# Performance work log

Measured on AMD Instinct MI355X. Metric: run time of the kernel, lower is better.

## Reference

```python
import jax, jax.numpy as jnp
import numpy as np

N, C, H, W = 64, 256, 28, 28
INTER = 128  # in_channels // reduction
STD = 0.01   # init std of the 1x1 convs


def setup_inputs() -> dict:
    key = jax.random.key(0)
    k_x, k_idx, k_wq, k_wv, k_lam = jax.random.split(key, 5)
    x = jax.random.normal(k_x, (N, C, H, W), dtype=jnp.float32)
    lam = jax.random.uniform(k_lam, (), dtype=jnp.float32)
    index = jax.random.randint(k_idx, (N,), 0, N)
    # query 1x1 conv (shared for q and k since x_qk_concat=False -> key is None)
    Wq = jax.random.normal(k_wq, (INTER, C), dtype=jnp.float32) * STD
    bq = jnp.zeros((INTER,), dtype=jnp.float32)
    # value 1x1 conv -> 1 channel
    Wv = jax.random.normal(k_wv, (1, C), dtype=jnp.float32) * STD
    bv = jnp.zeros((1,), dtype=jnp.float32)
    return {"x": x, "lam": lam, "index": index, "Wq": Wq, "bq": bq,
            "Wv": Wv, "bv": bv, "scale_factor": 8}


def _conv1x1(x, w, b):
    # x: [n,c,h,w], w: [o,c], b: [o] -> [n,o,h,w]
    return jnp.einsum('nchw,oc->nohw', x, w) + b[None, :, None, None]


def reference(x, lam, index, Wq, bq, Wv, bv, scale_factor):
    n, c, h, w = x.shape
    hw = h * w
    x_lam = x               # [n,c,h,w]
    x_lam_ = x[index]       # shuffled pair
    # value: 1x1 conv to 1 channel -> [n, hw, 1]
    v = _conv1x1(x_lam_, Wv, bv).reshape(n, 1, hw).transpose(0, 2, 1)
    # query / key share the same conv (key is None when x_qk_concat=False)
    q = _conv1x1(x_lam, Wq, bq).reshape(n, INTER, hw).transpose(0, 2, 1)  # [n,hw,inter]
    k = _conv1x1(x_lam_, Wq, bq).reshape(n, INTER, hw)                    # [n,inter,hw]
    # embedded gaussian similarity, forced fp32, scaled by sqrt(inter)
    scores = jnp.einsum('nqc,nck->nqk', q.astype(jnp.float32), k.astype(jnp.float32))
    scores = scores / jnp.float32(np.sqrt(INTER))
    pw = jax.nn.softmax(scores, axis=-1)  # [n,hw,hw]
    mask = jnp.einsum('nqk,nko->nqo', pw, v.astype(jnp.float32)).reshape(n, 1, h, w)
    # bilinear upsample (align_corners=False semantics) then sigmoid
    mask = jax.image.resize(mask, (n, 1, h * scale_factor, w * scale_factor),
                            method='bilinear')
    mask = jax.nn.sigmoid(mask)
    # results['mask'] = cat([1 - m, m], dim=1)
    return jnp.concatenate([1.0 - mask, mask], axis=1)
```

## Files before the change

### kernel.cpp

```cpp
#include <hip/hip_runtime.h>
#include <math.h>

#define NB    64
#define CIN   256
#define HH    28
#define WW    28
#define HW    784
#define INTER 128

typedef __bf16 bf16x8 __attribute__((ext_vector_type(8)));
typedef float  f32x4  __attribute__((ext_vector_type(4)));

#define SCALE 0.29730177875068026f

#define GLB(p) ((const __attribute__((address_space(1))) void*)(p))
#define LDSP(p) ((__attribute__((address_space(3))) void*)(p))

__device__ __forceinline__ unsigned int bfbits(float f) {
    unsigned int u = __builtin_bit_cast(unsigned int, f);
    return (u + 0x7fffu + ((u >> 16) & 1u)) >> 16;
}

__global__ __launch_bounds__(256) void initw_kernel(
    const float* __restrict__ Wq, unsigned short* __restrict__ Wbh)
{
    const int e  = blockIdx.x * 256 + threadIdx.x;
    const int j  = e & 7;
    const int l  = (e >> 3) & 63;
    const int it = (e >> 9) & 7;
    const int s  = e >> 12;
    const int i  = it * 16 + (l & 15);
    const int c  = s * 32 + ((l >> 4) & 3) * 8 + j;
    Wbh[e] = (unsigned short)bfbits(Wq[i * CIN + c] * SCALE);
}

__global__ __launch_bounds__(256, 5) void proj_kernel(
    const float* __restrict__ x,
    const unsigned short* __restrict__ Wfh,
    const float* __restrict__ bq,
    const float* __restrict__ Wv, const float* __restrict__ bv,
    unsigned short* __restrict__ Yb, float* __restrict__ vAll)
{
    __shared__ float          Xs [2][32 * 64];
    __shared__ unsigned short Whs[2][4096];

    const int ptile = blockIdx.x;
    const int n     = blockIdx.y;
    const int t     = threadIdx.x;
    const int l     = t & 63;
    const int w     = t >> 6;
    const int pl    = l & 15;
    const int g     = l >> 4;
    const int p0    = ptile * 64;

    const float* xn = x + (size_t)n * (CIN * HW);

    const int kk    = pl ^ (w << 2);
    const int psrc  = min(p0 + kk * 4, HW - 4);

    const int slot  = ((w * 16 + pl) >> 2) ^ (g << 2);
    const int rbyte = slot * 4 + (pl & 3);

    f32x4 acc[8];
#pragma unroll
    for (int it = 0; it < 8; ++it) acc[it] = (f32x4){0.f, 0.f, 0.f, 0.f};
    float vpart = 0.0f;

#pragma unroll
    for (int q = 0; q < 2; ++q) {
        const int rt = w * 8 + q * 4 + g;
        __builtin_amdgcn_global_load_lds(GLB(xn + (size_t)rt * HW + psrc),
                                         LDSP(&Xs[0][(w * 8 + q * 4) * 64]), 16, 0, 0);
        const int chunk = (w * 2 + q) * 512;
        __builtin_amdgcn_global_load_lds(GLB(Wfh + chunk + l * 8),
                                         LDSP(&Whs[0][chunk]), 16, 0, 0);
    }
    __syncthreads();

    int cur = 0;
    for (int s = 0; s < 8; ++s) {
        if (s < 7) {
#pragma unroll
            for (int q = 0; q < 2; ++q) {
                const int rt = w * 8 + q * 4 + g;
                __builtin_amdgcn_global_load_lds(
                    GLB(xn + (size_t)((s + 1) * 32 + rt) * HW + psrc),
                    LDSP(&Xs[cur ^ 1][(w * 8 + q * 4) * 64]), 16, 0, 0);
                const int chunk = (w * 2 + q) * 512;
                __builtin_amdgcn_global_load_lds(
                    GLB(Wfh + (s + 1) * 4096 + chunk + l * 8),
                    LDSP(&Whs[cur ^ 1][chunk]), 16, 0, 0);
            }
        }

        float xv[8];
#pragma unroll
        for (int j = 0; j < 8; ++j)
            xv[j] = Xs[cur][(g * 8 + j) * 64 + rbyte];

        const float4 wv0 = *(const float4*)(Wv + s * 32 + g * 8);
        const float4 wv1 = *(const float4*)(Wv + s * 32 + g * 8 + 4);
        vpart = fmaf(xv[0], wv0.x, fmaf(xv[1], wv0.y,
                fmaf(xv[2], wv0.z, fmaf(xv[3], wv0.w, vpart))));
        vpart = fmaf(xv[4], wv1.x, fmaf(xv[5], wv1.y,
                fmaf(xv[6], wv1.z, fmaf(xv[7], wv1.w, vpart))));

        bf16x8 ah;
#pragma unroll
        for (int j = 0; j < 8; ++j) ah[j] = (__bf16)xv[j];

#pragma unroll
        for (int it = 0; it < 8; ++it) {
            const bf16x8 wh = *(const bf16x8*)&Whs[cur][it * 512 + l * 8];
            acc[it] = __builtin_amdgcn_mfma_f32_16x16x32_bf16(ah, wh, acc[it], 0, 0, 0);
        }

        __syncthreads();
        cur ^= 1;
    }

    const int p0w = p0 + w * 16;

    vpart += __shfl_xor(vpart, 16);
    vpart += __shfl_xor(vpart, 32);
    if (g == 0 && p0w + pl < HW)
        vAll[n * HW + p0w + pl] = vpart + bv[0];

#pragma unroll
    for (int it = 0; it < 8; ++it) {
        const int i = it * 16 + pl;
        const float bb = bq[i] * SCALE;
#pragma unroll
        for (int r = 0; r < 4; ++r) {
            const int pr = p0w + g * 4 + r;
            if (pr < HW)
                Yb[((size_t)n * HW + pr) * INTER + i] =
                    (unsigned short)bfbits(acc[it][r] + bb);
        }
    }
}

__global__ __launch_bounds__(256) void attn_kernel(
    const unsigned short* __restrict__ Yb, const float* __restrict__ vAll,
    const int* __restrict__ index, float* __restrict__ maskbuf)
{
    __shared__ float red[2][4][64];

    const int qt  = blockIdx.x;
    const int n   = blockIdx.y;
    const int q0  = qt * 64;
    const int t   = threadIdx.x;
    const int l   = t & 63;
    const int w   = t >> 6;
    const int idx = index[n];

    const unsigned short* Qg = Yb + (size_t)n   * (HW * INTER);
    const unsigned short* Kg = Yb + (size_t)idx * (HW * INTER);
    const float*          Vg = vAll + (size_t)idx * HW;

    const int ql = l & 15;
    const int g  = l >> 4;

    bf16x8 qf[4][4];
#pragma unroll
    for (int qg = 0; qg < 4; ++qg) {
        const int qrow = min(q0 + qg * 16 + ql, HW - 1);
#pragma unroll
        for (int ic = 0; ic < 4; ++ic)
            qf[qg][ic] = *(const bf16x8*)(Qg + (size_t)qrow * INTER + ic * 32 + g * 8);
    }

    float ll[4] = {0.f, 0.f, 0.f, 0.f};
    float oo[4] = {0.f, 0.f, 0.f, 0.f};

    const int NT = (w == 0) ? 13 : 12;
    const unsigned short* Ka = Kg + (size_t)(w * 16 + ql) * INTER + g * 8;
    const float*          Va = Vg + w * 16 + g * 4;

    bf16x8 afA[4], afB[4];
    float4 vvA, vvB;

#define LOADK(kt, dst, vdst)                                               \
    {                                                                      \
        const unsigned short* kp = Ka + (size_t)(kt) * (64 * INTER);       \
        dst[0] = *(const bf16x8*)(kp);                                     \
        dst[1] = *(const bf16x8*)(kp + 32);                                \
        dst[2] = *(const bf16x8*)(kp + 64);                                \
        dst[3] = *(const bf16x8*)(kp + 96);                                \
        vdst = *(const float4*)(Va + (kt) * 64);                           \
    }

#define PROCESS(af, vv)                                                    \
    {                                                                      \
        _Pragma("unroll")                                                  \
        for (int qg = 0; qg < 4; ++qg) {                                   \
            f32x4 acc = (f32x4){0.f, 0.f, 0.f, 0.f};                       \
            _Pragma("unroll")                                              \
            for (int ic = 0; ic < 4; ++ic)                                 \
                acc = __builtin_amdgcn_mfma_f32_16x16x32_bf16(             \
                    af[ic], qf[qg][ic], acc, 0, 0, 0);                     \
            const float e0 = __expf(acc[0]);                               \
            const float e1 = __expf(acc[1]);                               \
            const float e2 = __expf(acc[2]);                               \
            const float e3 = __expf(acc[3]);                               \
            ll[qg] += (e0 + e1) + (e2 + e3);                               \
            oo[qg] = fmaf(e0, vv.x, fmaf(e1, vv.y,                         \
                     fmaf(e2, vv.z, fmaf(e3, vv.w, oo[qg]))));             \
        }                                                                  \
    }

    LOADK(0, afA, vvA);
    int kt = 0;
    for (; kt + 1 < NT; kt += 2) {
        LOADK(kt + 1, afB, vvB);
        PROCESS(afA, vvA);
        if (kt + 2 < NT) LOADK(kt + 2, afA, vvA);
        PROCESS(afB, vvB);
    }
    if (kt < NT) PROCESS(afA, vvA);

#undef LOADK
#undef PROCESS

#pragma unroll
    for (int qg = 0; qg < 4; ++qg) {
        ll[qg] += __shfl_xor(ll[qg], 16); ll[qg] += __shfl_xor(ll[qg], 32);
        oo[qg] += __shfl_xor(oo[qg], 16); oo[qg] += __shfl_xor(oo[qg], 32);
    }
    if (g == 0) {
#pragma unroll
        for (int qg = 0; qg < 4; ++qg) {
            red[0][w][qg * 16 + ql] = ll[qg];
            red[1][w][qg * 16 + ql] = oo[qg];
        }
    }
    __syncthreads();
    if (t < 64 && q0 + t < HW) {
        const float L = red[0][0][t] + red[0][1][t] + red[0][2][t] + red[0][3][t];
        const float O = red[1][0][t] + red[1][1][t] + red[1][2][t] + red[1][3][t];
        maskbuf[n * HW + q0 + t] = O / L;
    }
}

__global__ __launch_bounds__(256) void upsample_kernel(
    const float* __restrict__ maskbuf, float* __restrict__ out)
{
    const int gid = blockIdx.x * 256 + threadIdx.x;
    const int n  = gid / (224 * 56);
    const int r  = gid - n * (224 * 56);
    const int oy = r / 56;
    const int xq = r - oy * 56;

    const float iy = (oy + 0.5f) * 0.125f - 0.5f;
    const int   y0 = (int)floorf(iy);
    const float fy = iy - (float)y0;
    const int y0c = max(y0, 0), y1c = min(y0 + 1, HH - 1);
    const float* mrow = maskbuf + n * HW;

    float res[4];
#pragma unroll
    for (int j = 0; j < 4; ++j) {
        const int   ox = (xq << 2) + j;
        const float ix = (ox + 0.5f) * 0.125f - 0.5f;
        const int   x0 = (int)floorf(ix);
        const float fx = ix - (float)x0;
        const int x0c = max(x0, 0), x1c = min(x0 + 1, WW - 1);
        const float v00 = mrow[y0c * WW + x0c], v01 = mrow[y0c * WW + x1c];
        const float v10 = mrow[y1c * WW + x0c], v11 = mrow[y1c * WW + x1c];
        const float m = (v00 * (1.0f - fx) + v01 * fx) * (1.0f - fy)
                      + (v10 * (1.0f - fx) + v11 * fx) * fy;
        res[j] = 1.0f / (1.0f + __expf(-m));
    }

    float4 pos = make_float4(res[0], res[1], res[2], res[3]);
    float4 neg = make_float4(1.0f - res[0], 1.0f - res[1],
                             1.0f - res[2], 1.0f - res[3]);
    const size_t base = (size_t)n * 2 * 50176 + (size_t)oy * 224 + (xq << 2);
    *(float4*)(out + base)         = neg;
    *(float4*)(out + base + 50176) = pos;
}

extern "C" void kernel_launch(void* const* d_in, const int* in_sizes, int n_in,
                              void* d_out, int out_size, void* d_ws, size_t ws_size,
                              hipStream_t stream) {
    const float* x     = (const float*)d_in[0];
    const int*   index = (const int*)d_in[2];
    const float* Wq    = (const float*)d_in[3];
    const float* bq    = (const float*)d_in[4];
    const float* Wv    = (const float*)d_in[5];
    const float* bv    = (const float*)d_in[6];

    float* out = (float*)d_out;
    unsigned short* Yb  = (unsigned short*)d_out;
    unsigned short* Wbh = Yb + (size_t)NB * HW * INTER;
    float* vAll  = (float*)d_ws;
    float* maskb = vAll + NB * HW;

    initw_kernel<<<128, 256, 0, stream>>>(Wq, Wbh);
    proj_kernel<<<dim3(13, NB), 256, 0, stream>>>(
        x, Wbh, bq, Wv, bv, Yb, vAll);
    attn_kernel<<<dim3(13, NB), 256, 0, stream>>>(Yb, vAll, index, maskb);
    upsample_kernel<<<3136, 256, 0, stream>>>(maskb, out);
}
```

Before: 67.40 us.

## Load x columns directly into registers and stage weights in two halves

The projection kernel no longer double-buffers x tiles through LDS over 8 pipelined steps. Each thread now loads all 64 of its x values straight from global memory into registers up front. The bf16 weights are staged into LDS in two 32KB halves, the second half loading while the first four MFMA steps run. This drops most of the barriers and the x-through-LDS traffic. In exchange it uses far more registers and LDS (launch bounds relaxed, so occupancy may fall) and the scalar strided global loads may coalesce less well.

```diff
diff --git a/kernel.cpp b/kernel.cpp
--- a/kernel.cpp
+++ b/kernel.cpp
@@ -34,15 +34,14 @@
     Wbh[e] = (unsigned short)bfbits(Wq[i * CIN + c] * SCALE);
 }
 
-__global__ __launch_bounds__(256, 5) void proj_kernel(
+__global__ __launch_bounds__(256) void proj_kernel(
     const float* __restrict__ x,
     const unsigned short* __restrict__ Wfh,
     const float* __restrict__ bq,
     const float* __restrict__ Wv, const float* __restrict__ bv,
     unsigned short* __restrict__ Yb, float* __restrict__ vAll)
 {
-    __shared__ float          Xs [2][32 * 64];
-    __shared__ unsigned short Whs[2][4096];
+    __shared__ unsigned short Whs[2][16384];
 
     const int ptile = blockIdx.x;
     const int n     = blockIdx.y;
@@ -51,75 +50,57 @@
     const int w     = t >> 6;
     const int pl    = l & 15;
     const int g     = l >> 4;
-    const int p0    = ptile * 64;
-
-    const float* xn = x + (size_t)n * (CIN * HW);
-
-    const int kk    = pl ^ (w << 2);
-    const int psrc  = min(p0 + kk * 4, HW - 4);
-
-    const int slot  = ((w * 16 + pl) >> 2) ^ (g << 2);
-    const int rbyte = slot * 4 + (pl & 3);
+    const int p0w   = ptile * 64 + w * 16;
+
+    const int pa = min(p0w + pl, HW - 1);
+    const float* xcol = x + (size_t)n * (CIN * HW) + pa;
+
+#pragma unroll
+    for (int q = 0; q < 8; ++q)
+        __builtin_amdgcn_global_load_lds(GLB(Wfh + (q * 256 + t) * 8),
+                                         LDSP(&Whs[0][(q * 256 + t) * 8]), 16, 0, 0);
+
+    float xv[8][8];
+#pragma unroll
+    for (int s = 0; s < 8; ++s)
+#pragma unroll
+        for (int j = 0; j < 8; ++j)
+            xv[s][j] = xcol[(size_t)(s * 32 + g * 8 + j) * HW];
+
+    __syncthreads();
+
+#pragma unroll
+    for (int q = 0; q < 8; ++q)
+        __builtin_amdgcn_global_load_lds(GLB(Wfh + 16384 + (q * 256 + t) * 8),
+                                         LDSP(&Whs[1][(q * 256 + t) * 8]), 16, 0, 0);
 
     f32x4 acc[8];
 #pragma unroll
     for (int it = 0; it < 8; ++it) acc[it] = (f32x4){0.f, 0.f, 0.f, 0.f};
     float vpart = 0.0f;
 
-#pragma unroll
-    for (int q = 0; q < 2; ++q) {
-        const int rt = w * 8 + q * 4 + g;
-        __builtin_amdgcn_global_load_lds(GLB(xn + (size_t)rt * HW + psrc),
-                                         LDSP(&Xs[0][(w * 8 + q * 4) * 64]), 16, 0, 0);
-        const int chunk = (w * 2 + q) * 512;
-        __builtin_amdgcn_global_load_lds(GLB(Wfh + chunk + l * 8),
-                                         LDSP(&Whs[0][chunk]), 16, 0, 0);
-    }
+#define PSTEP(s, h, so)                                                        \
+    {                                                                          \
+        const float4 wv0 = *(const float4*)(Wv + (s) * 32 + g * 8);            \
+        const float4 wv1 = *(const float4*)(Wv + (s) * 32 + g * 8 + 4);        \
+        vpart = fmaf(xv[s][0], wv0.x, fmaf(xv[s][1], wv0.y,                    \
+                fmaf(xv[s][2], wv0.z, fmaf(xv[s][3], wv0.w, vpart))));         \
+        vpart = fmaf(xv[s][4], wv1.x, fmaf(xv[s][5], wv1.y,                    \
+                fmaf(xv[s][6], wv1.z, fmaf(xv[s][7], wv1.w, vpart))));         \
+        bf16x8 ah;                                                             \
+        _Pragma("unroll")                                                      \
+        for (int j = 0; j < 8; ++j) ah[j] = (__bf16)xv[s][j];                  \
+        _Pragma("unroll")                                                      \
+        for (int it = 0; it < 8; ++it) {                                       \
+            const bf16x8 wh = *(const bf16x8*)&Whs[h][(so) * 4096 + it * 512 + l * 8]; \
+            acc[it] = __builtin_amdgcn_mfma_f32_16x16x32_bf16(ah, wh, acc[it], 0, 0, 0); \
+        }                                                                      \
+    }
+
+    PSTEP(0, 0, 0) PSTEP(1, 0, 1) PSTEP(2, 0, 2) PSTEP(3, 0, 3)
     __syncthreads();
-
-    int cur = 0;
-    for (int s = 0; s < 8; ++s) {
-        if (s < 7) {
-#pragma unroll
-            for (int q = 0; q < 2; ++q) {
-                const int rt = w * 8 + q * 4 + g;
-                __builtin_amdgcn_global_load_lds(
-                    GLB(xn + (size_t)((s + 1) * 32 + rt) * HW + psrc),
-                    LDSP(&Xs[cur ^ 1][(w * 8 + q * 4) * 64]), 16, 0, 0);
-                const int chunk = (w * 2 + q) * 512;
-                __builtin_amdgcn_global_load_lds(
-                    GLB(Wfh + (s + 1) * 4096 + chunk + l * 8),
-                    LDSP(&Whs[cur ^ 1][chunk]), 16, 0, 0);
-            }
-        }
-
-        float xv[8];
-#pragma unroll
-        for (int j = 0; j < 8; ++j)
-            xv[j] = Xs[cur][(g * 8 + j) * 64 + rbyte];
-
-        const float4 wv0 = *(const float4*)(Wv + s * 32 + g * 8);
-        const float4 wv1 = *(const float4*)(Wv + s * 32 + g * 8 + 4);
-        vpart = fmaf(xv[0], wv0.x, fmaf(xv[1], wv0.y,
-                fmaf(xv[2], wv0.z, fmaf(xv[3], wv0.w, vpart))));
-        vpart = fmaf(xv[4], wv1.x, fmaf(xv[5], wv1.y,
-                fmaf(xv[6], wv1.z, fmaf(xv[7], wv1.w, vpart))));
-
-        bf16x8 ah;
-#pragma unroll
-        for (int j = 0; j < 8; ++j) ah[j] = (__bf16)xv[j];
-
-#pragma unroll
-        for (int it = 0; it < 8; ++it) {
-            const bf16x8 wh = *(const bf16x8*)&Whs[cur][it * 512 + l * 8];
-            acc[it] = __builtin_amdgcn_mfma_f32_16x16x32_bf16(ah, wh, acc[it], 0, 0, 0);
-        }
-
-        __syncthreads();
-        cur ^= 1;
-    }
-
-    const int p0w = p0 + w * 16;
+    PSTEP(4, 1, 0) PSTEP(5, 1, 1) PSTEP(6, 1, 2) PSTEP(7, 1, 3)
+#undef PSTEP
 
     vpart += __shfl_xor(vpart, 16);
     vpart += __shfl_xor(vpart, 32);
```

New measurement: 71.11 us. 1.05x slower.
